# Kernel optimization log

Measured on AMD Instinct MI355X. Metric: run time of the kernel, lower is better.

Reference implementation:

```python
import jax, jax.numpy as jnp
import numpy as np

B, T, HID = 1, 2048, 2048
H = 16            # num_heads == num_key_value_heads
D = HID // H      # head_dim == feature_dim == 128
EPS = 1e-5


def _layer_norm(x, eps=1e-5):
    mu = jnp.mean(x, axis=-1, keepdims=True)
    var = jnp.mean((x - mu) ** 2, axis=-1, keepdims=True)
    return (x - mu) * jax.lax.rsqrt(var + eps)


def _feature_map(x, gamma, beta):
    # ReBased feature map, flatten=False (parallel mode): affine then LayerNorm
    return _layer_norm(x * gamma + beta)


def setup_inputs() -> dict:
    key = jax.random.key(0)
    ks = jax.random.split(key, 8)
    s = HID ** -0.5
    return {
        "hidden_states": jax.random.normal(ks[0], (B, T, HID), jnp.float32),
        "Wq": jax.random.normal(ks[1], (HID, HID), jnp.float32) * s,
        "Wk": jax.random.normal(ks[2], (HID, HID), jnp.float32) * s,
        "Wv": jax.random.normal(ks[3], (HID, HID), jnp.float32) * s,
        "Wo": jax.random.normal(ks[4], (HID, HID), jnp.float32) * s,
        "gamma": 1.0 + 0.1 * jax.random.normal(ks[5], (D,), jnp.float32),
        "beta": 0.1 * jax.random.normal(ks[6], (D,), jnp.float32),
    }


def reference(hidden_states, Wq, Wk, Wv, Wo, gamma, beta):
    b, t, _ = hidden_states.shape
    # projections (nn.Linear: x @ W.T), split into heads: [b, t, h, d]
    q = (hidden_states @ Wq.T).reshape(b, t, H, D)
    k = (hidden_states @ Wk.T).reshape(b, t, H, D)
    v = (hidden_states @ Wv.T).reshape(b, t, H, D)
    # ReBased feature map (no quadratic flatten in parallel mode)
    q = _feature_map(q, gamma, beta)
    k = _feature_map(k, gamma, beta)
    # parallel_rebased: scale q, quadratic score, causal mask, normalize
    q = q * (D ** -0.5)
    attn = jnp.einsum('bqhd,bkhd->bhqk', q, k) ** 2  # (q.k)^2
    mask = jnp.tril(jnp.ones((t, t), dtype=bool))
    attn = jnp.where(mask, attn, 0.0)
    o = jnp.einsum('bhqk,bkhd->bqhd', attn, v)       # [b, t, h, d]
    z = jnp.sum(attn, axis=-1)                       # [b, h, t]
    o = o / (jnp.swapaxes(z, 1, 2)[..., None] + EPS)
    o = o.reshape(b, t, H * D)
    return o @ Wo.T
```

## Files before the change

### kernel.cpp

```cpp
#include <hip/hip_runtime.h>
#include <hip/hip_bf16.h>
#include <stdint.h>

typedef __bf16 bf16;
typedef __bf16 v8bf __attribute__((ext_vector_type(8)));
typedef __bf16 v4bf __attribute__((ext_vector_type(4)));
typedef float  v4f  __attribute__((ext_vector_type(4)));

#define TSEQ   2048
#define HIDDIM 2048
#define NHEAD  16
#define HDIM   128

__device__ __forceinline__ void async16(void* lds, const void* g)
{
    __builtin_amdgcn_global_load_lds(
        (__attribute__((address_space(1))) void*)(uintptr_t)g,
        (__attribute__((address_space(3))) void*)(unsigned int)(uintptr_t)lds,
        16, 0, 0);
}

__global__ __launch_bounds__(256) void conv5(const float* __restrict__ s0, bf16* __restrict__ d0,
                                             const float* __restrict__ s1, bf16* __restrict__ d1,
                                             const float* __restrict__ s2, bf16* __restrict__ d2,
                                             const float* __restrict__ s3, bf16* __restrict__ d3,
                                             const float* __restrict__ s4, bf16* __restrict__ d4)
{
    const float* src; bf16* dst;
    switch (blockIdx.y) {
        case 0: src = s0; dst = d0; break;
        case 1: src = s1; dst = d1; break;
        case 2: src = s2; dst = d2; break;
        case 3: src = s3; dst = d3; break;
        default: src = s4; dst = d4; break;
    }
    const size_t i = ((size_t)blockIdx.x * 256 + threadIdx.x) * 8;
    const float4 a = *(const float4*)(src + i);
    const float4 b = *(const float4*)(src + i + 4);
    v8bf o;
    o[0] = (bf16)a.x; o[1] = (bf16)a.y; o[2] = (bf16)a.z; o[3] = (bf16)a.w;
    o[4] = (bf16)b.x; o[5] = (bf16)b.y; o[6] = (bf16)b.z; o[7] = (bf16)b.w;
    *(v8bf*)(dst + i) = o;
}


#define PBAR() do { __builtin_amdgcn_sched_barrier(0); __builtin_amdgcn_s_barrier(); \
                    __builtin_amdgcn_sched_barrier(0); } while (0)

#define STU(ldst, gsrc) do { \
    async16((ldst) + w*512,        (gsrc) + (size_t)(w*8 + (l>>3))*2048); \
    async16((ldst) + 4096 + w*512, (gsrc) + (size_t)(64 + w*8 + (l>>3))*2048); \
} while (0)

#define RDA(buf) do { _Pragma("unroll") \
    for (int mi_ = 0; mi_ < 4; ++mi_) { \
        const bf16* p_ = &sA[(buf)*8192 + (wm*64 + mi_*16 + lr)*64]; \
        a[mi_][0] = *(const v8bf*)(p_ + c0); \
        a[mi_][1] = *(const v8bf*)(p_ + c1); } } while (0)

#define RDB(buf, nh) do { _Pragma("unroll") \
    for (int nj_ = 0; nj_ < 2; ++nj_) { \
        const bf16* p_ = &sB[(buf)*24576 + ((nh)*128 + wn*32 + nj_*16 + lr)*64]; \
        b[nj_][0] = *(const v8bf*)(p_ + c0); \
        b[nj_][1] = *(const v8bf*)(p_ + c1); } } while (0)

#define MQ(nh) do { _Pragma("unroll") \
    for (int mi_ = 0; mi_ < 4; ++mi_) { _Pragma("unroll") \
        for (int nj_ = 0; nj_ < 2; ++nj_) { \
            acc[mi_][(nh)*2+nj_] = __builtin_amdgcn_mfma_f32_16x16x32_bf16( \
                a[mi_][0], b[nj_][0], acc[mi_][(nh)*2+nj_], 0, 0, 0); \
            acc[mi_][(nh)*2+nj_] = __builtin_amdgcn_mfma_f32_16x16x32_bf16( \
                a[mi_][1], b[nj_][1], acc[mi_][(nh)*2+nj_], 0, 0, 0); \
        } } } while (0)

#define VMC(n) asm volatile("s_waitcnt vmcnt(" #n ")" ::: "memory")

__global__ __launch_bounds__(512, 2) void gemm_qkv384(const bf16* __restrict__ A,
    const bf16* __restrict__ Wcat, bf16* __restrict__ qb, bf16* __restrict__ kb,
    bf16* __restrict__ vt, const float* __restrict__ gamma, const float* __restrict__ beta)
{
    __shared__ __attribute__((aligned(16))) bf16 sA[2*8192];
    __shared__ __attribute__((aligned(16))) bf16 sB[2*24576];
    const int n0g = blockIdx.x * 384;
    const int m0  = blockIdx.y * 128;

    const int tid = threadIdx.x, l = tid & 63, w = tid >> 6;
    const int wm = w >> 2, wn = w & 3;
    const int quad = l >> 4, lr = l & 15;
    const int scol = ((l & 7) ^ ((l >> 3) & 7)) * 8;
    const int c0 = ((quad    ) ^ (lr & 7)) * 8;
    const int c1 = ((quad + 4) ^ (lr & 7)) * 8;

    const bf16* Ag = A    + (size_t)m0  * 2048 + scol;
    const bf16* Bg = Wcat + (size_t)n0g * 2048 + scol;

    v4f  acc[4][6] = {};
    v8bf a[4][2], b[2][2];

    STU(&sA[0],           Ag);
    STU(&sB[0],           Bg);
    STU(&sB[8192],        Bg + (size_t)128*2048);
    STU(&sB[16384],       Bg + (size_t)256*2048);
    STU(&sA[8192],        Ag + 64);
    STU(&sB[24576],       Bg + 64);
    STU(&sB[24576+8192],  Bg + (size_t)128*2048 + 64);
    VMC(10);
    __builtin_amdgcn_s_barrier();
    __builtin_amdgcn_sched_barrier(0);

#pragma unroll 1
    for (int it = 0; it < 16; ++it) {
        const int k1 =  it*128 + 64;
        const int k2 = (it*128 + 128) & 2047;
        const int k3 = (it*128 + 192) & 2047;

        RDA(0); RDB(0, 0);
        STU(&sB[24576+16384], Bg + (size_t)256*2048 + k1);
        PBAR(); __builtin_amdgcn_s_setprio(1); MQ(0); __builtin_amdgcn_s_setprio(0);
        VMC(10); PBAR();
        RDB(0, 1);
        STU(&sA[0], Ag + k2);
        STU(&sB[0], Bg + k2);
        PBAR(); __builtin_amdgcn_s_setprio(1); MQ(1); __builtin_amdgcn_s_setprio(0);
        VMC(12); PBAR();
        RDB(0, 2);
        STU(&sB[8192], Bg + (size_t)128*2048 + k2);
        PBAR(); __builtin_amdgcn_s_setprio(1); MQ(2); __builtin_amdgcn_s_setprio(0);
        VMC(10); PBAR();
        RDA(1); RDB(1, 0);
        STU(&sB[16384], Bg + (size_t)256*2048 + k2);
        PBAR(); __builtin_amdgcn_s_setprio(1); MQ(0); __builtin_amdgcn_s_setprio(0);
        VMC(10); PBAR();
        RDB(1, 1);
        STU(&sA[8192],  Ag + k3);
        STU(&sB[24576], Bg + k3);
        PBAR(); __builtin_amdgcn_s_setprio(1); MQ(1); __builtin_amdgcn_s_setprio(0);
        VMC(12); PBAR();
        RDB(1, 2);
        STU(&sB[24576+8192], Bg + (size_t)128*2048 + k3);
        PBAR(); __builtin_amdgcn_s_setprio(1); MQ(2); __builtin_amdgcn_s_setprio(0);
        VMC(10); PBAR();
    }
    asm volatile("s_waitcnt vmcnt(0)" ::: "memory");
    __syncthreads();

    float* sRed = (float*)sA;
    const float g0f = gamma[wn*32 + lr],      b0f = beta[wn*32 + lr];
    const float g1f = gamma[wn*32 + 16 + lr], b1f = beta[wn*32 + 16 + lr];

#pragma unroll
    for (int nh = 0; nh < 3; ++nh) {
        if (((n0g + nh*128) >> 11) == 2) continue;
#pragma unroll
        for (int mi = 0; mi < 4; ++mi) {
            float s[4] = {0.f,0.f,0.f,0.f}, sq[4] = {0.f,0.f,0.f,0.f};
#pragma unroll
            for (int jj = 0; jj < 2; ++jj) {
                const float gg = jj ? g1f : g0f, bb = jj ? b1f : b0f;
#pragma unroll
                for (int r = 0; r < 4; ++r) {
                    float x = acc[mi][nh*2+jj][r] * gg + bb;
                    acc[mi][nh*2+jj][r] = x;
                    s[r] += x; sq[r] += x*x;
                }
            }
#pragma unroll
            for (int off = 1; off < 16; off <<= 1)
#pragma unroll
                for (int r = 0; r < 4; ++r) {
                    s[r]  += __shfl_xor(s[r],  off);
                    sq[r] += __shfl_xor(sq[r], off);
                }
            if (lr == 0) {
#pragma unroll
                for (int r = 0; r < 4; ++r) {
                    const int row = wm*64 + mi*16 + quad*4 + r;
                    float* p = &sRed[((nh*128 + row)*5 + wn)*2];
                    p[0] = s[r]; p[1] = sq[r];
                }
            }
        }
    }
    __syncthreads();

#pragma unroll
    for (int mi = 0; mi < 4; ++mi) {
        const int row = m0 + wm*64 + mi*16 + quad*4;
        const int rl0 = wm*64 + mi*16 + quad*4;
#pragma unroll
        for (int nh = 0; nh < 3; ++nh) {
            const int colg  = n0g + nh*128 + wn*32;
            const int which = colg >> 11;
            if (which == 2) {
#pragma unroll
                for (int jj = 0; jj < 2; ++jj) {
                    const int c = (colg & 2047) + jj*16 + lr;
                    v4bf pk;
#pragma unroll
                    for (int r = 0; r < 4; ++r) pk[r] = (bf16)acc[mi][nh*2+jj][r];
                    *(v4bf*)(vt + (size_t)c*2048 + row) = pk;
                }
            } else {
                bf16* Cb = (which == 0) ? qb : kb;
                const float qs = (which == 0) ? 0.08838834764831845f : 1.0f;
#pragma unroll
                for (int r = 0; r < 4; ++r) {
                    const int rl = rl0 + r;
                    float S = 0.f, Q = 0.f;
#pragma unroll
                    for (int t = 0; t < 4; ++t) {
                        const float* p = &sRed[((nh*128 + rl)*5 + t)*2];
                        S += p[0]; Q += p[1];
                    }
                    const float mu = S * (1.0f/128.0f);
                    float var = Q * (1.0f/128.0f) - mu*mu;
                    var = fmaxf(var, 0.0f);
                    const float rstd = rsqrtf(var + 1e-5f) * qs;
#pragma unroll
                    for (int jj = 0; jj < 2; ++jj) {
                        const int lcol = (colg & 2047) + jj*16 + lr;
                        Cb[(size_t)(row + r)*2048 + lcol] =
                            (bf16)((acc[mi][nh*2+jj][r] - mu) * rstd);
                    }
                }
            }
        }
    }
}

__global__ __launch_bounds__(256) void gemm_out(const bf16* __restrict__ A,
    const bf16* __restrict__ B, float* __restrict__ C)
{
    __shared__ __attribute__((aligned(16))) bf16 sA[128*32];
    __shared__ __attribute__((aligned(16))) bf16 sB[64*32];
    const int m0 = blockIdx.y * 128, n0 = blockIdx.x * 64;
    const int K = HIDDIM, ldc = HIDDIM;
    const int tid  = threadIdx.x;
    const int lane = tid & 63;
    const int w    = tid >> 6;
    const int wm   = w >> 1, wn = w & 1;
    const int quad = lane >> 4, lr = lane & 15;
    const int srow = lane >> 2;
    const int scol = (lane & 3) * 8;

    const bf16* gA0 = A + (size_t)(m0 + w*32 + srow) * K + scol;
    const bf16* gB0 = B + (size_t)(n0 + w*16 + srow) * K + scol;
    bf16* lA0 = &sA[w*1024];
    bf16* lB0 = &sB[w*512];

    v4f acc[4][2] = {};

    for (int kt = 0; kt < K; kt += 32) {
        __syncthreads();
        async16(lA0,       gA0 + kt);
        async16(lA0 + 512, gA0 + (size_t)16*K + kt);
        async16(lB0,       gB0 + kt);
        __syncthreads();
        v8bf a[4], b[2];
#pragma unroll
        for (int i = 0; i < 4; ++i)
            a[i] = *(const v8bf*)&sA[(wm*64 + i*16 + lr)*32 + quad*8];
#pragma unroll
        for (int j = 0; j < 2; ++j)
            b[j] = *(const v8bf*)&sB[(wn*32 + j*16 + lr)*32 + quad*8];
#pragma unroll
        for (int i = 0; i < 4; ++i)
#pragma unroll
            for (int j = 0; j < 2; ++j)
                acc[i][j] = __builtin_amdgcn_mfma_f32_16x16x32_bf16(a[i], b[j], acc[i][j], 0, 0, 0);
    }

#pragma unroll
    for (int i = 0; i < 4; ++i) {
        const int row_b = m0 + wm*64 + i*16 + quad*4;
#pragma unroll
        for (int j = 0; j < 2; ++j) {
            const int col = n0 + wn*32 + j*16 + lr;
#pragma unroll
            for (int r = 0; r < 4; ++r)
                C[(size_t)(row_b + r)*ldc + col] = acc[i][j][r];
        }
    }
}

__global__ __launch_bounds__(512, 2) void attn(const bf16* __restrict__ qb,
                                               const bf16* __restrict__ kb,
                                               const bf16* __restrict__ vt,
                                               bf16* __restrict__ ob)
{
    __shared__ __attribute__((aligned(16))) bf16 sK[2*64*136];
    __shared__ __attribute__((aligned(16))) bf16 sV[2*128*72];
    __shared__ __attribute__((aligned(16))) bf16 sS[2*64*72];
    __shared__ __attribute__((aligned(16))) float sO[64*129];
    __shared__ __attribute__((aligned(16))) float sZ[64*17];

    const int h    = blockIdx.y;
    const int pr   = blockIdx.x;
    const int tid  = threadIdx.x, lane = tid & 63;
    const int w    = tid >> 6;
    const int g    = w >> 2;
    const int ww   = w & 3;
    const int quad = lane >> 4, lr = lane & 15;
    const int rs   = tid >> 4;
    const int cs   = (tid & 15) * 8;

#pragma unroll
    for (int ti = 0; ti < 2; ++ti) {
        const int tile = ti ? pr : (31 - pr);
        const int nch  = tile + 1;

        v8bf qa[4];
        {
            const bf16* q0 = qb + (size_t)(tile*64 + ww*16 + lr)*HIDDIM + h*HDIM + quad*8;
#pragma unroll
            for (int ks = 0; ks < 4; ++ks)
                qa[ks] = *(const v8bf*)(q0 + ks*32);
        }

        v4f  o[8] = {};
        float z[4] = {0.f, 0.f, 0.f, 0.f};

        v8bf curK[4], curV[4], nxtK[4], nxtV[4];
#pragma unroll
        for (int p = 0; p < 4; ++p) {
            curK[p] = *(const v8bf*)(kb + (size_t)(rs + p*32)*HIDDIM + h*HDIM + cs);
            curV[p] = *(const v8bf*)(vt + (size_t)(h*HDIM + rs + p*32)*HIDDIM + cs);
        }

        for (int ich = 0; ich < nch; ich += 2) {
            __syncthreads();
#pragma unroll
            for (int p = 0; p < 4; ++p) {
                const int r = rs + p*32;
                *(v8bf*)&sK[(r>>6)*8704 + (r&63)*136 + cs] = curK[p];
            }
#pragma unroll
            for (int p = 0; p < 4; ++p)
                *(v8bf*)&sV[(cs>>6)*9216 + (rs + p*32)*72 + (cs & 63)] = curV[p];

            if (ich + 2 < nch) {
                const int s1 = (ich + 2) * 64;
#pragma unroll
                for (int p = 0; p < 4; ++p) {
                    nxtK[p] = *(const v8bf*)(kb + (size_t)(s1 + rs + p*32)*HIDDIM + h*HDIM + cs);
                    nxtV[p] = *(const v8bf*)(vt + (size_t)(h*HDIM + rs + p*32)*HIDDIM + s1 + cs);
                }
            }
            __syncthreads();

            const int ch = ich + g;
            if (ch < nch) {
                const bf16* sKg = &sK[g*8704];
                const bf16* sVg = &sV[g*9216];
                bf16*       sSg = &sS[g*4608];
                const bool  diag = (ch == tile);
                const int   s0   = ch * 64;

                v8bf kbf[4][4];
#pragma unroll
                for (int nj = 0; nj < 4; ++nj)
#pragma unroll
                    for (int ks = 0; ks < 4; ++ks)
                        kbf[nj][ks] = *(const v8bf*)&sKg[(nj*16 + lr)*136 + ks*32 + quad*8];
                const int row_l = ww*16 + quad*4;
                const int qg    = tile*64 + row_l;
#pragma unroll
                for (int nj = 0; nj < 4; ++nj) {
                    v4f s4 = {0.f, 0.f, 0.f, 0.f};
#pragma unroll
                    for (int ks = 0; ks < 4; ++ks)
                        s4 = __builtin_amdgcn_mfma_f32_16x16x32_bf16(qa[ks], kbf[nj][ks], s4, 0, 0, 0);
                    const int col = nj*16 + lr;
                    const int sg  = s0 + col;
#pragma unroll
                    for (int r = 0; r < 4; ++r) {
                        float val = s4[r] * s4[r];
                        if (diag && (sg > qg + r)) val = 0.0f;
                        const bf16 vb16 = (bf16)val;
                        z[r] += (float)vb16;
                        sSg[(row_l + r)*72 + col] = vb16;
                    }
                }

#pragma unroll
                for (int ks = 0; ks < 2; ++ks) {
                    const v8bf sa = *(const v8bf*)&sSg[(ww*16 + lr)*72 + ks*32 + quad*8];
#pragma unroll
                    for (int nd = 0; nd < 8; ++nd) {
                        const v8bf vbf = *(const v8bf*)&sVg[(nd*16 + lr)*72 + ks*32 + quad*8];
                        o[nd] = __builtin_amdgcn_mfma_f32_16x16x32_bf16(sa, vbf, o[nd], 0, 0, 0);
                    }
                }
            }

            if (ich + 2 < nch) {
#pragma unroll
                for (int p = 0; p < 4; ++p) { curK[p] = nxtK[p]; curV[p] = nxtV[p]; }
            }
        }

        const int row_l = ww*16 + quad*4;
        __syncthreads();
        if (g == 1) {
#pragma unroll
            for (int nd = 0; nd < 8; ++nd)
#pragma unroll
                for (int r = 0; r < 4; ++r)
                    sO[(row_l + r)*129 + nd*16 + lr] = o[nd][r];
#pragma unroll
            for (int r = 0; r < 4; ++r)
                sZ[(row_l + r)*17 + lr] = z[r];
        }
        __syncthreads();
        if (g == 0) {
#pragma unroll
            for (int nd = 0; nd < 8; ++nd)
#pragma unroll
                for (int r = 0; r < 4; ++r)
                    o[nd][r] += sO[(row_l + r)*129 + nd*16 + lr];
#pragma unroll
            for (int r = 0; r < 4; ++r) {
                float zz = z[r] + sZ[(row_l + r)*17 + lr];
                zz += __shfl_xor(zz, 1); zz += __shfl_xor(zz, 2);
                zz += __shfl_xor(zz, 4); zz += __shfl_xor(zz, 8);
                z[r] = zz + 1e-5f;
            }
            const size_t rbase = (size_t)(tile*64 + row_l)*HIDDIM + h*HDIM;
#pragma unroll
            for (int nd = 0; nd < 8; ++nd) {
                const int col = nd*16 + lr;
#pragma unroll
                for (int r = 0; r < 4; ++r)
                    ob[rbase + (size_t)r*HIDDIM + col] = (bf16)(o[nd][r] / z[r]);
            }
        }
    }
}

extern "C" void kernel_launch(void* const* d_in, const int* in_sizes, int n_in,
                              void* d_out, int out_size, void* d_ws, size_t ws_size,
                              hipStream_t stream)
{
    const float* hs    = (const float*)d_in[0];
    const float* Wq    = (const float*)d_in[1];
    const float* Wk    = (const float*)d_in[2];
    const float* Wv    = (const float*)d_in[3];
    const float* Wo    = (const float*)d_in[4];
    const float* gamma = (const float*)d_in[5];
    const float* beta  = (const float*)d_in[6];
    float* outp = (float*)d_out;

    const size_t MAT = (size_t)TSEQ * HIDDIM;

    bf16* ws   = (bf16*)d_ws;
    bf16* hs_b = ws + 0*MAT;
    bf16* ob   = hs_b;
    bf16* Wq_b = ws + 1*MAT;
    bf16* Wk_b = ws + 2*MAT;
    bf16* Wv_b = ws + 3*MAT;
    bf16* Wo_b = ws + 4*MAT;
    bf16* vt   = ws + 5*MAT;
    bf16* qb   = (bf16*)d_out;
    bf16* kb   = (bf16*)d_out + MAT;

    conv5<<<dim3(2048, 5), 256, 0, stream>>>(hs, hs_b, Wq, Wq_b, Wk, Wk_b, Wv, Wv_b, Wo, Wo_b);
    gemm_qkv384<<<dim3(16, 16), 512, 0, stream>>>(hs_b, Wq_b, qb, kb, vt, gamma, beta);
    attn<<<dim3(16, 16), 512, 0, stream>>>(qb, kb, vt, ob);
    gemm_out<<<dim3(32, 16), 256, 0, stream>>>(ob, Wo_b, outp);
}
```

Baseline: 266.8 us.

## Stage QK projection tiles in LDS for row-wise LayerNorm and vectorized stores

The LayerNorm epilogue of the fused QKV projection GEMM now writes each 128-column head tile as bf16 into shared memory. Each group of four threads then reads one row, computes mean and variance with two shuffles, and writes 16-byte vector stores. The old version did cross-lane shuffle reductions, a shared-memory partial-sum exchange, and scattered 2-byte global stores. The tile now passes through bf16 before normalization, which loses some precision, and each head tile adds two barriers.

```diff
diff --git a/kernel.cpp b/kernel.cpp
--- a/kernel.cpp
+++ b/kernel.cpp
@@ -141,89 +141,78 @@
         PBAR(); __builtin_amdgcn_s_setprio(1); MQ(2); __builtin_amdgcn_s_setprio(0);
         VMC(10); PBAR();
     }
-    asm volatile("s_waitcnt vmcnt(0)" ::: "memory");
+    VMC(0);
     __syncthreads();
 
-    float* sRed = (float*)sA;
-    const float g0f = gamma[wn*32 + lr],      b0f = beta[wn*32 + lr];
-    const float g1f = gamma[wn*32 + 16 + lr], b1f = beta[wn*32 + 16 + lr];
+    bf16* sT = sB;
+    const int erow = tid >> 2;
+    const int ecol = (tid & 3) * 32;
+    float gv[32], bv[32];
+#pragma unroll
+    for (int i = 0; i < 8; ++i) {
+        *(float4*)&gv[i*4] = *(const float4*)(gamma + ecol + i*4);
+        *(float4*)&bv[i*4] = *(const float4*)(beta  + ecol + i*4);
+    }
 
 #pragma unroll
     for (int nh = 0; nh < 3; ++nh) {
-        if (((n0g + nh*128) >> 11) == 2) continue;
-#pragma unroll
-        for (int mi = 0; mi < 4; ++mi) {
-            float s[4] = {0.f,0.f,0.f,0.f}, sq[4] = {0.f,0.f,0.f,0.f};
-#pragma unroll
-            for (int jj = 0; jj < 2; ++jj) {
-                const float gg = jj ? g1f : g0f, bb = jj ? b1f : b0f;
-#pragma unroll
-                for (int r = 0; r < 4; ++r) {
-                    float x = acc[mi][nh*2+jj][r] * gg + bb;
-                    acc[mi][nh*2+jj][r] = x;
-                    s[r] += x; sq[r] += x*x;
-                }
-            }
-#pragma unroll
-            for (int off = 1; off < 16; off <<= 1)
-#pragma unroll
-                for (int r = 0; r < 4; ++r) {
-                    s[r]  += __shfl_xor(s[r],  off);
-                    sq[r] += __shfl_xor(sq[r], off);
-                }
-            if (lr == 0) {
-#pragma unroll
-                for (int r = 0; r < 4; ++r) {
-                    const int row = wm*64 + mi*16 + quad*4 + r;
-                    float* p = &sRed[((nh*128 + row)*5 + wn)*2];
-                    p[0] = s[r]; p[1] = sq[r];
-                }
-            }
-        }
-    }
-    __syncthreads();
-
-#pragma unroll
-    for (int mi = 0; mi < 4; ++mi) {
-        const int row = m0 + wm*64 + mi*16 + quad*4;
-        const int rl0 = wm*64 + mi*16 + quad*4;
-#pragma unroll
-        for (int nh = 0; nh < 3; ++nh) {
-            const int colg  = n0g + nh*128 + wn*32;
-            const int which = colg >> 11;
-            if (which == 2) {
+        const int colg0 = n0g + nh*128;
+        const int which = colg0 >> 11;
+        if (which == 2) {
+#pragma unroll
+            for (int mi = 0; mi < 4; ++mi) {
+                const int row = m0 + wm*64 + mi*16 + quad*4;
 #pragma unroll
                 for (int jj = 0; jj < 2; ++jj) {
-                    const int c = (colg & 2047) + jj*16 + lr;
+                    const int c = (colg0 & 2047) + wn*32 + jj*16 + lr;
                     v4bf pk;
 #pragma unroll
                     for (int r = 0; r < 4; ++r) pk[r] = (bf16)acc[mi][nh*2+jj][r];
                     *(v4bf*)(vt + (size_t)c*2048 + row) = pk;
                 }
-            } else {
-                bf16* Cb = (which == 0) ? qb : kb;
-                const float qs = (which == 0) ? 0.08838834764831845f : 1.0f;
-#pragma unroll
-                for (int r = 0; r < 4; ++r) {
-                    const int rl = rl0 + r;
-                    float S = 0.f, Q = 0.f;
-#pragma unroll
-                    for (int t = 0; t < 4; ++t) {
-                        const float* p = &sRed[((nh*128 + rl)*5 + t)*2];
-                        S += p[0]; Q += p[1];
-                    }
-                    const float mu = S * (1.0f/128.0f);
-                    float var = Q * (1.0f/128.0f) - mu*mu;
-                    var = fmaxf(var, 0.0f);
-                    const float rstd = rsqrtf(var + 1e-5f) * qs;
-#pragma unroll
-                    for (int jj = 0; jj < 2; ++jj) {
-                        const int lcol = (colg & 2047) + jj*16 + lr;
-                        Cb[(size_t)(row + r)*2048 + lcol] =
-                            (bf16)((acc[mi][nh*2+jj][r] - mu) * rstd);
-                    }
-                }
-            }
+            }
+        } else {
+#pragma unroll
+            for (int mi = 0; mi < 4; ++mi) {
+                const int row = wm*64 + mi*16 + quad*4;
+#pragma unroll
+                for (int jj = 0; jj < 2; ++jj) {
+                    const int col = wn*32 + jj*16 + lr;
+#pragma unroll
+                    for (int r = 0; r < 4; ++r)
+                        sT[(row + r)*136 + col] = (bf16)acc[mi][nh*2+jj][r];
+                }
+            }
+            __syncthreads();
+            float x[32];
+            float s = 0.f, q = 0.f;
+#pragma unroll
+            for (int i = 0; i < 4; ++i) {
+                const v8bf v = *(const v8bf*)&sT[erow*136 + ecol + i*8];
+#pragma unroll
+                for (int k = 0; k < 8; ++k) {
+                    const float xv = (float)v[k] * gv[i*8+k] + bv[i*8+k];
+                    x[i*8+k] = xv; s += xv; q += xv*xv;
+                }
+            }
+            s += __shfl_xor(s, 1); q += __shfl_xor(q, 1);
+            s += __shfl_xor(s, 2); q += __shfl_xor(q, 2);
+            const float mu = s * (1.0f/128.0f);
+            float var = q * (1.0f/128.0f) - mu*mu;
+            var = fmaxf(var, 0.0f);
+            bf16* Cb = (which == 0) ? qb : kb;
+            const float qs = (which == 0) ? 0.08838834764831845f : 1.0f;
+            const float rstd = rsqrtf(var + 1e-5f) * qs;
+            bf16* dst = Cb + (size_t)(m0 + erow)*2048 + (colg0 & 2047) + ecol;
+#pragma unroll
+            for (int i = 0; i < 4; ++i) {
+                v8bf o;
+#pragma unroll
+                for (int k = 0; k < 8; ++k)
+                    o[k] = (bf16)((x[i*8+k] - mu) * rstd);
+                *(v8bf*)(dst + i*8) = o;
+            }
+            __syncthreads();
         }
     }
 }
```

Measured after the change: 260.3 us. -2.4%, faster.
